# Kernel tuning notes

Hardware: AMD Instinct MI355X
Metric: run time of the kernel (lower is better)

## Reference

```python
import jax, jax.numpy as jnp
import numpy as np


def setup_inputs() -> dict:
    key = jax.random.key(0)
    k1, k2, k3, k4, k5 = jax.random.split(key, 5)
    B, S, I, H = 64, 2048, 512, 512
    scale = 1.0 / np.sqrt(H)
    return {
        "x": jax.random.normal(k1, (B, S, I), dtype=jnp.float32),
        "h0": jax.random.normal(k2, (B, H), dtype=jnp.float32),
        "Wx": jax.random.normal(k3, (H, I), dtype=jnp.float32) * scale,
        "Wh": jax.random.normal(k4, (H, H), dtype=jnp.float32) * scale,
        "bh": jax.random.normal(k5, (H,), dtype=jnp.float32) * scale,
    }


def reference(x, h0, Wx, Wh, bh):
    # Precompute input projection for all timesteps as one big GEMM:
    # (B,S,I) @ (I,H) -> (B,S,H)
    xproj = jnp.einsum("bsi,hi->bsh", x, Wx)

    def step(h, xp_t):
        # h: (B,H), xp_t: (B,H)
        h_new = jnp.tanh(xp_t + h @ Wh.T + bh)
        return h_new, h_new

    # scan over time axis: move seq to leading dim (S,B,H)
    h_last, outs = jax.lax.scan(step, h0, jnp.swapaxes(xproj, 0, 1))
    outputs = jnp.swapaxes(outs, 0, 1)  # (B,S,H)
    return outputs, h_last
```

## Files before the change

### kernel.cpp

```cpp
#include <hip/hip_runtime.h>
#include <cmath>

#define BB 64
#define SS 2048
#define II 512
#define HH 512

__global__ __launch_bounds__(256) void xproj_kernel(
    const float* __restrict__ A,
    const float* __restrict__ W,
    const float* __restrict__ bias,
    float* __restrict__ C)
{
    __shared__ float Ast[16][68];
    __shared__ float Bst[16][68];

    const int tid = threadIdx.x;
    const long m0 = (long)blockIdx.x * 64;
    const int n0 = blockIdx.y * 64;
    const int row = tid >> 2;
    const int kq = (tid & 3) << 2;
    const int tx = tid & 15;
    const int ty = tid >> 4;

    float acc[4][4] = {};

    for (int k0 = 0; k0 < 512; k0 += 16) {
        float4 a4 = *(const float4*)&A[(m0 + row) * 512 + k0 + kq];
        float4 b4 = *(const float4*)&W[(long)(n0 + row) * 512 + k0 + kq];
        __syncthreads();
        Ast[kq + 0][row] = a4.x; Ast[kq + 1][row] = a4.y;
        Ast[kq + 2][row] = a4.z; Ast[kq + 3][row] = a4.w;
        Bst[kq + 0][row] = b4.x; Bst[kq + 1][row] = b4.y;
        Bst[kq + 2][row] = b4.z; Bst[kq + 3][row] = b4.w;
        __syncthreads();
#pragma unroll
        for (int kk = 0; kk < 16; ++kk) {
            float4 av = *(const float4*)&Ast[kk][ty << 2];
            float4 bv = *(const float4*)&Bst[kk][tx << 2];
            acc[0][0] += av.x * bv.x; acc[0][1] += av.x * bv.y;
            acc[0][2] += av.x * bv.z; acc[0][3] += av.x * bv.w;
            acc[1][0] += av.y * bv.x; acc[1][1] += av.y * bv.y;
            acc[1][2] += av.y * bv.z; acc[1][3] += av.y * bv.w;
            acc[2][0] += av.z * bv.x; acc[2][1] += av.z * bv.y;
            acc[2][2] += av.z * bv.z; acc[2][3] += av.z * bv.w;
            acc[3][0] += av.w * bv.x; acc[3][1] += av.w * bv.y;
            acc[3][2] += av.w * bv.z; acc[3][3] += av.w * bv.w;
        }
    }

    float4 bias4 = *(const float4*)&bias[n0 + (tx << 2)];
#pragma unroll
    for (int a = 0; a < 4; ++a) {
        float4 o;
        o.x = acc[a][0] + bias4.x;
        o.y = acc[a][1] + bias4.y;
        o.z = acc[a][2] + bias4.z;
        o.w = acc[a][3] + bias4.w;
        *(float4*)&C[(m0 + (ty << 2) + a) * 512 + n0 + (tx << 2)] = o;
    }
}

__global__ __launch_bounds__(256) void transpose512(
    const float* __restrict__ in, float* __restrict__ out)
{
    __shared__ float tile[32][33];
    int x = blockIdx.x * 32 + threadIdx.x;
    int y = blockIdx.y * 32 + threadIdx.y;
#pragma unroll
    for (int i = 0; i < 32; i += 8)
        tile[threadIdx.y + i][threadIdx.x] = in[(y + i) * 512 + x];
    __syncthreads();
    x = blockIdx.y * 32 + threadIdx.x;
    y = blockIdx.x * 32 + threadIdx.y;
#pragma unroll
    for (int i = 0; i < 32; i += 8)
        out[(y + i) * 512 + x] = tile[threadIdx.x][threadIdx.y + i];
}

#define REP32(M) M(0) M(1) M(2) M(3) M(4) M(5) M(6) M(7) \
                 M(8) M(9) M(10) M(11) M(12) M(13) M(14) M(15) \
                 M(16) M(17) M(18) M(19) M(20) M(21) M(22) M(23) \
                 M(24) M(25) M(26) M(27) M(28) M(29) M(30) M(31)

__global__ __launch_bounds__(512, 1) void rnn_coop(
    float* __restrict__ out,
    const float* __restrict__ WhT,
    const float* __restrict__ h0,
    float* __restrict__ hlast,
    unsigned long long* __restrict__ hbuf)
{
    __shared__ float hsh[HH];
    __shared__ float psum[512];

    const int bid = blockIdx.x;
    const int b   = bid >> 2;
    const int s   = bid & 3;
    const int j0  = s * 128;
    const int tid = threadIdx.x;
    const int q   = tid >> 7;
    const int jl  = tid & 127;
    const int j   = j0 + jl;
    const int kb  = q * 128;

    const float* wsrc = WhT + (long)kb * HH + j;
#define DECLW(i) float4 wr##i; \
    wr##i.x = wsrc[(4*(i)+0)*HH]; wr##i.y = wsrc[(4*(i)+1)*HH]; \
    wr##i.z = wsrc[(4*(i)+2)*HH]; wr##i.w = wsrc[(4*(i)+3)*HH];
    REP32(DECLW)
#undef DECLW
#define PINW(i) asm volatile("" : "+v"(wr##i.x), "+v"(wr##i.y), \
                                  "+v"(wr##i.z), "+v"(wr##i.w));
    REP32(PINW)
#undef PINW

    hsh[tid] = h0[b * HH + tid];
    __syncthreads();

    float* po = out + (long)b * SS * HH + j;
    float xpv = 0.f;
    if (tid < 128) xpv = po[0];

    for (int t = 0; t < SS; ++t) {
        float xpn = 0.f;
        if (tid < 128 && t + 1 < SS) xpn = po[(long)(t + 1) * HH];

        float a0 = 0.f, a1 = 0.f, a2 = 0.f, a3 = 0.f;
#define FMAW(i) { float4 hv = *(const float4*)&hsh[kb + 4*(i)]; \
        a0 = fmaf(wr##i.x, hv.x, a0); a1 = fmaf(wr##i.y, hv.y, a1); \
        a2 = fmaf(wr##i.z, hv.z, a2); a3 = fmaf(wr##i.w, hv.w, a3); }
        REP32(FMAW)
#undef FMAW
        psum[tid] = (a0 + a1) + (a2 + a3);
        __syncthreads();

        const int par = (t + 1) & 1;
        unsigned long long* slot = hbuf + (long)par * (BB * HH) + b * HH;

        if (tid < 128) {
            float v = psum[tid] + psum[tid + 128] + psum[tid + 256] +
                      psum[tid + 384] + xpv;
            float hn = tanhf(v);
            hsh[j0 + tid] = hn;
            po[(long)t * HH] = hn;
            unsigned long long pk =
                ((unsigned long long)(unsigned)(t + 1) << 32) |
                (unsigned long long)__float_as_uint(hn);
            __hip_atomic_store(&slot[j0 + tid], pk,
                               __ATOMIC_RELAXED, __HIP_MEMORY_SCOPE_AGENT);
        } else {
            int fj = tid - 128;
            int jg = fj + (fj >= j0 ? 128 : 0);
            unsigned long long pk;
            do {
                pk = __hip_atomic_load(&slot[jg], __ATOMIC_RELAXED,
                                       __HIP_MEMORY_SCOPE_AGENT);
            } while ((int)(pk >> 32) != t + 1);
            hsh[jg] = __uint_as_float((unsigned)pk);
        }
        __syncthreads();
        xpv = xpn;
    }

    if (s == 0) hlast[b * HH + tid] = hsh[tid];
}

template <bool TRANS>
__global__ __launch_bounds__(512) void rnn_kernel(
    float* __restrict__ out,
    const float* __restrict__ Whx,
    const float* __restrict__ h0,
    float* __restrict__ hlast)
{
    __shared__ float h[HH];
    const int b = blockIdx.x;
    const int j = threadIdx.x;

    h[j] = h0[b * HH + j];
    __syncthreads();

    float* po = out + (long)b * SS * HH + j;

    for (int t = 0; t < SS; ++t) {
        float acc = po[(long)t * HH];
#pragma unroll 4
        for (int k = 0; k < HH; k += 4) {
            float4 hv = *(const float4*)&h[k];
            if (TRANS) {
                acc += Whx[(k + 0) * HH + j] * hv.x;
                acc += Whx[(k + 1) * HH + j] * hv.y;
                acc += Whx[(k + 2) * HH + j] * hv.z;
                acc += Whx[(k + 3) * HH + j] * hv.w;
            } else {
                acc += Whx[j * HH + (k + 0)] * hv.x;
                acc += Whx[j * HH + (k + 1)] * hv.y;
                acc += Whx[j * HH + (k + 2)] * hv.z;
                acc += Whx[j * HH + (k + 3)] * hv.w;
            }
        }
        float hn = tanhf(acc);
        __syncthreads();
        h[j] = hn;
        po[(long)t * HH] = hn;
        __syncthreads();
    }

    hlast[b * HH + j] = h[j];
}

extern "C" void kernel_launch(void* const* d_in, const int* in_sizes, int n_in,
                              void* d_out, int out_size, void* d_ws, size_t ws_size,
                              hipStream_t stream) {
    const float* x  = (const float*)d_in[0];
    const float* h0 = (const float*)d_in[1];
    const float* Wx = (const float*)d_in[2];
    const float* Wh = (const float*)d_in[3];
    const float* bh = (const float*)d_in[4];

    float* out = (float*)d_out;
    float* hlast = out + (long)BB * SS * HH;

    dim3 gA(BB * SS / 64, HH / 64);
    xproj_kernel<<<gA, 256, 0, stream>>>(x, Wx, bh, out);

    const size_t whBytes   = (size_t)HH * HH * sizeof(float);
    const size_t hbufBytes = (size_t)2 * BB * HH * sizeof(unsigned long long);

    if (ws_size >= whBytes + hbufBytes) {
        float* WhT = (float*)d_ws;
        unsigned long long* hbuf = (unsigned long long*)((char*)d_ws + whBytes);

        transpose512<<<dim3(16, 16), dim3(32, 8), 0, stream>>>(Wh, WhT);
        hipMemsetAsync(hbuf, 0, hbufBytes, stream);

        void* args[] = {(void*)&out, (void*)&WhT, (void*)&h0, (void*)&hlast,
                        (void*)&hbuf};
        hipError_t ce = hipLaunchCooperativeKernel(
            (const void*)rnn_coop, dim3(BB * 4), dim3(512), args, 0, stream);
        if (ce != hipSuccess) {
            (void)hipGetLastError();
            rnn_kernel<true><<<BB, HH, 0, stream>>>(out, WhT, h0, hlast);
        }
    } else if (ws_size >= whBytes) {
        float* WhT = (float*)d_ws;
        transpose512<<<dim3(16, 16), dim3(32, 8), 0, stream>>>(Wh, WhT);
        rnn_kernel<true><<<BB, HH, 0, stream>>>(out, WhT, h0, hlast);
    } else {
        rnn_kernel<false><<<BB, HH, 0, stream>>>(out, Wh, h0, hlast);
    }
}
```

Baseline: 4.998 ms.

## Add dual-buffer fast polling path for inter-block hidden state exchange

Adds a second exchange buffer that producers also write with a plain volatile store. Consumers poll it with an inline-asm global load using the sc0 cache bit, and fall back to the agent-scope atomic buffer every 256 iterations or when the first step shows the fast path is not seen. The block-to-batch mapping is also changed so the four slices of one batch are spread across block IDs, which likely places them on different XCDs or CUs. The aim is to cut the latency of the per-timestep cross-block spin-wait. The risk is stale or incoherent reads if sc0 does not bypass the right cache level, which the fallback is meant to cover.

```diff
diff --git a/kernel.cpp b/kernel.cpp
--- a/kernel.cpp
+++ b/kernel.cpp
@@ -83,19 +83,31 @@
                  M(16) M(17) M(18) M(19) M(20) M(21) M(22) M(23) \
                  M(24) M(25) M(26) M(27) M(28) M(29) M(30) M(31)
 
+__device__ __forceinline__ unsigned long long fast_poll_ld(
+    const unsigned long long* p) {
+    unsigned long long v;
+    asm volatile("global_load_dwordx2 %0, %1, off sc0\n\t"
+                 "s_waitcnt vmcnt(0)"
+                 : "=v"(v) : "v"(p) : "memory");
+    return v;
+}
+
+template <bool DUAL>
 __global__ __launch_bounds__(512, 1) void rnn_coop(
     float* __restrict__ out,
     const float* __restrict__ WhT,
     const float* __restrict__ h0,
     float* __restrict__ hlast,
-    unsigned long long* __restrict__ hbuf)
+    unsigned long long* __restrict__ hbufS,
+    unsigned long long* __restrict__ hbufF)
 {
     __shared__ float hsh[HH];
     __shared__ float psum[512];
+    __shared__ int useF;
 
     const int bid = blockIdx.x;
-    const int b   = bid >> 2;
-    const int s   = bid & 3;
+    const int b   = bid & 63;
+    const int s   = bid >> 6;
     const int j0  = s * 128;
     const int tid = threadIdx.x;
     const int q   = tid >> 7;
@@ -115,6 +127,7 @@
 #undef PINW
 
     hsh[tid] = h0[b * HH + tid];
+    if (tid == 0) useF = DUAL ? 1 : 0;
     __syncthreads();
 
     float* po = out + (long)b * SS * HH + j;
@@ -135,7 +148,10 @@
         __syncthreads();
 
         const int par = (t + 1) & 1;
-        unsigned long long* slot = hbuf + (long)par * (BB * HH) + b * HH;
+        const long base = (long)par * (BB * HH) + b * HH;
+        unsigned long long* slotS = hbufS + base;
+        unsigned long long* slotF = DUAL ? hbufF + base : nullptr;
+        const int fastOn = DUAL ? useF : 0;
 
         if (tid < 128) {
             float v = psum[tid] + psum[tid + 128] + psum[tid + 256] +
@@ -146,16 +162,41 @@
             unsigned long long pk =
                 ((unsigned long long)(unsigned)(t + 1) << 32) |
                 (unsigned long long)__float_as_uint(hn);
-            __hip_atomic_store(&slot[j0 + tid], pk,
+            __hip_atomic_store(&slotS[j0 + tid], pk,
                                __ATOMIC_RELAXED, __HIP_MEMORY_SCOPE_AGENT);
+            if (DUAL)
+                *(volatile unsigned long long*)&slotF[j0 + tid] = pk;
         } else {
             int fj = tid - 128;
             int jg = fj + (fj >= j0 ? 128 : 0);
             unsigned long long pk;
-            do {
-                pk = __hip_atomic_load(&slot[jg], __ATOMIC_RELAXED,
-                                       __HIP_MEMORY_SCOPE_AGENT);
-            } while ((int)(pk >> 32) != t + 1);
+            if (DUAL && t == 0) {
+                bool fok = false;
+                for (;;) {
+                    unsigned long long pkF = fast_poll_ld(&slotF[jg]);
+                    if ((int)(pkF >> 32) == t + 1) { pk = pkF; fok = true; break; }
+                    pk = __hip_atomic_load(&slotS[jg], __ATOMIC_RELAXED,
+                                           __HIP_MEMORY_SCOPE_AGENT);
+                    if ((int)(pk >> 32) == t + 1) break;
+                }
+                if (!fok) useF = 0;
+            } else if (DUAL && fastOn) {
+                int it = 0;
+                for (;;) {
+                    unsigned long long pkF = fast_poll_ld(&slotF[jg]);
+                    if ((int)(pkF >> 32) == t + 1) { pk = pkF; break; }
+                    if (((++it) & 255) == 0) {
+                        pk = __hip_atomic_load(&slotS[jg], __ATOMIC_RELAXED,
+                                               __HIP_MEMORY_SCOPE_AGENT);
+                        if ((int)(pk >> 32) == t + 1) break;
+                    }
+                }
+            } else {
+                do {
+                    pk = __hip_atomic_load(&slotS[jg], __ATOMIC_RELAXED,
+                                           __HIP_MEMORY_SCOPE_AGENT);
+                } while ((int)(pk >> 32) != t + 1);
+            }
             hsh[jg] = __uint_as_float((unsigned)pk);
         }
         __syncthreads();
@@ -223,20 +264,37 @@
     dim3 gA(BB * SS / 64, HH / 64);
     xproj_kernel<<<gA, 256, 0, stream>>>(x, Wx, bh, out);
 
-    const size_t whBytes   = (size_t)HH * HH * sizeof(float);
-    const size_t hbufBytes = (size_t)2 * BB * HH * sizeof(unsigned long long);
-
-    if (ws_size >= whBytes + hbufBytes) {
+    const size_t whBytes  = (size_t)HH * HH * sizeof(float);
+    const size_t bufBytes = (size_t)2 * BB * HH * sizeof(unsigned long long);
+
+    if (ws_size >= whBytes + 2 * bufBytes) {
         float* WhT = (float*)d_ws;
-        unsigned long long* hbuf = (unsigned long long*)((char*)d_ws + whBytes);
+        unsigned long long* hbufS = (unsigned long long*)((char*)d_ws + whBytes);
+        unsigned long long* hbufF = (unsigned long long*)((char*)d_ws + whBytes + bufBytes);
 
         transpose512<<<dim3(16, 16), dim3(32, 8), 0, stream>>>(Wh, WhT);
-        hipMemsetAsync(hbuf, 0, hbufBytes, stream);
+        hipMemsetAsync(hbufS, 0, 2 * bufBytes, stream);
 
         void* args[] = {(void*)&out, (void*)&WhT, (void*)&h0, (void*)&hlast,
-                        (void*)&hbuf};
+                        (void*)&hbufS, (void*)&hbufF};
         hipError_t ce = hipLaunchCooperativeKernel(
-            (const void*)rnn_coop, dim3(BB * 4), dim3(512), args, 0, stream);
+            (const void*)rnn_coop<true>, dim3(BB * 4), dim3(512), args, 0, stream);
+        if (ce != hipSuccess) {
+            (void)hipGetLastError();
+            rnn_kernel<true><<<BB, HH, 0, stream>>>(out, WhT, h0, hlast);
+        }
+    } else if (ws_size >= whBytes + bufBytes) {
+        float* WhT = (float*)d_ws;
+        unsigned long long* hbufS = (unsigned long long*)((char*)d_ws + whBytes);
+        unsigned long long* hbufF = nullptr;
+
+        transpose512<<<dim3(16, 16), dim3(32, 8), 0, stream>>>(Wh, WhT);
+        hipMemsetAsync(hbufS, 0, bufBytes, stream);
+
+        void* args[] = {(void*)&out, (void*)&WhT, (void*)&h0, (void*)&hlast,
+                        (void*)&hbufS, (void*)&hbufF};
+        hipError_t ce = hipLaunchCooperativeKernel(
+            (const void*)rnn_coop<false>, dim3(BB * 4), dim3(512), args, 0, stream);
         if (ce != hipSuccess) {
             (void)hipGetLastError();
             rnn_kernel<true><<<BB, HH, 0, stream>>>(out, WhT, h0, hlast);
```

New measurement: 16.38 ms. 228% more time.
